# Kernel optimization log

Measured on AMD Instinct MI355X. Metric: run time of the kernel, lower is better.

The kernel has to match this reference:

```python
import jax, jax.numpy as jnp
import numpy as np

HEAD_NUM = 16
MASK_FILL = 100000.0  # source uses +1e5 on masked entries (not -inf)


def setup_inputs() -> dict:
    key = jax.random.key(0)
    k1, k2, k3, k4, k5 = jax.random.split(key, 5)
    B, S, E = 2, 2048, 1024
    scale = 0.02
    return {
        "x": jax.random.normal(k1, (B, S, E), dtype=jnp.float32),
        "W_atten": jax.random.normal(k2, (E, 3 * E), dtype=jnp.float32) * scale,
        "b_atten": jax.random.normal(k3, (3 * E,), dtype=jnp.float32) * scale,
        "W_proj": jax.random.normal(k4, (E, E), dtype=jnp.float32) * scale,
        "b_proj": jax.random.normal(k5, (E,), dtype=jnp.float32) * scale,
    }


def reference(x, W_atten, b_atten, W_proj, b_proj):
    B, S, E = x.shape
    H = HEAD_NUM
    hd = E // H
    # QKV projection: [B, S, 3E]
    qkv = x @ W_atten + b_atten
    # reshape [B, S, H, 3*hd] -> [B, H, S, 3*hd], chunk into q,k,v [B,H,S,hd]
    qkv = jnp.transpose(qkv.reshape(B, S, H, 3 * hd), (0, 2, 1, 3))
    q, k, v = jnp.split(qkv, 3, axis=-1)
    # raw scores, NO 1/sqrt(dk) scaling (faithful to source)
    w = jnp.einsum("bhqd,bhkd->bhqk", q, k)
    # causal mask applied as w*mask + (1-mask)*1e5 (faithful to source)
    mask = jnp.tril(jnp.ones((S, S), dtype=w.dtype))
    w = w * mask + (1.0 - mask) * MASK_FILL
    # softmax over dim=1 == HEAD axis (faithful to source quirk)
    w = jax.nn.softmax(w, axis=1)
    # attn_drop: identity in eval mode
    a = jnp.einsum("bhqk,bhkd->bhqd", w, v)  # [B,H,S,hd]
    a = jnp.transpose(a, (0, 2, 1, 3)).reshape(B, S, E)
    h = a @ W_proj + b_proj
    # resi_drop: identity in eval mode
    return h
```

## Files before the change

### kernel.cpp

```cpp
#include <hip/hip_runtime.h>

#define DI __device__ __forceinline__

typedef __attribute__((ext_vector_type(8))) short s16x8;
typedef __attribute__((ext_vector_type(4))) short s16x4;
typedef __attribute__((ext_vector_type(4))) float f32x4;

DI unsigned short f2bf(float f){
  unsigned u = __float_as_uint(f);
  u = (u + 0x7FFFu + ((u >> 16) & 1u)) >> 16;
  return (unsigned short)u;
}
DI float bf2f(unsigned short h){
  return __uint_as_float(((unsigned)h) << 16);
}

DI void gll16(const void* g, void* l){
  __builtin_amdgcn_global_load_lds((const __attribute__((address_space(1))) void*)g,
                                   (__attribute__((address_space(3))) void*)l, 16, 0, 0);
}

__global__ void cvt_kernel(const float* __restrict__ in, unsigned short* __restrict__ out, int n8){
  int i = blockIdx.x * blockDim.x + threadIdx.x;
  if (i >= n8) return;
  const float4* p = (const float4*)in + (size_t)i * 2;
  float4 a = p[0], b = p[1];
  s16x8 o;
  o[0] = (short)f2bf(a.x); o[1] = (short)f2bf(a.y); o[2] = (short)f2bf(a.z); o[3] = (short)f2bf(a.w);
  o[4] = (short)f2bf(b.x); o[5] = (short)f2bf(b.y); o[6] = (short)f2bf(b.z); o[7] = (short)f2bf(b.w);
  ((s16x8*)out)[i] = o;
}

__global__ void transpose_cvt(const float* __restrict__ in, unsigned short* __restrict__ out, int R, int C){
  __shared__ float t[32][33];
  int c0 = blockIdx.x * 32, r0 = blockIdx.y * 32;
  int tx = threadIdx.x, ty = threadIdx.y;
  #pragma unroll
  for (int i = 0; i < 4; i++)
    t[ty + i*8][tx] = in[(size_t)(r0 + ty + i*8) * C + c0 + tx];
  __syncthreads();
  #pragma unroll
  for (int i = 0; i < 4; i++)
    out[(size_t)(c0 + ty + i*8) * R + r0 + tx] = f2bf(t[tx][ty + i*8]);
}

template<int MODE>
__launch_bounds__(256)
__global__ void gemm_kernel(const unsigned short* __restrict__ A,
                            const unsigned short* __restrict__ Wt,
                            const float* __restrict__ bias,
                            int N,
                            unsigned short* __restrict__ qb,
                            unsigned short* __restrict__ kb,
                            unsigned short* __restrict__ vt,
                            float* __restrict__ out)
{
  const int K = 1024;
  __shared__ unsigned short As[128 * 64];
  __shared__ unsigned short Bs[128 * 64];
  int m0 = blockIdx.y * 128, n0 = blockIdx.x * 128;
  int tid = threadIdx.x;
  int lane = tid & 63, w = tid >> 6;
  int row_l = lane & 15, kgrp = lane >> 4;
  int wm = (w >> 1) * 64, wn = (w & 1) * 64;

  const unsigned short* asrc[4];
  const unsigned short* bsrc[4];
  int ldso[4];
  int chunk = (lane & 7) ^ (lane >> 3);
  #pragma unroll
  for (int c4 = 0; c4 < 4; c4++){
    int r = c4*32 + w*8 + (lane >> 3);
    asrc[c4] = A  + (size_t)(m0 + r) * K + chunk*8;
    bsrc[c4] = Wt + (size_t)(n0 + r) * K + chunk*8;
    ldso[c4] = (c4*32 + w*8) * 64;
  }
  int eA[4], eB[4];
  #pragma unroll
  for (int i = 0; i < 4; i++){
    int ra = wm + i*16 + row_l;
    eA[i] = (ra*64 + kgrp*8) ^ ((ra & 7) << 3);
    int rb = wn + i*16 + row_l;
    eB[i] = (rb*64 + kgrp*8) ^ ((rb & 7) << 3);
  }

  f32x4 acc[4][4];
  #pragma unroll
  for (int i = 0; i < 4; i++)
    #pragma unroll
    for (int j = 0; j < 4; j++)
      acc[i][j] = (f32x4){0.f, 0.f, 0.f, 0.f};

  for (int k0 = 0; k0 < K; k0 += 64){
    #pragma unroll
    for (int c4 = 0; c4 < 4; c4++){
      gll16(asrc[c4] + k0, (void*)(As + ldso[c4]));
      gll16(bsrc[c4] + k0, (void*)(Bs + ldso[c4]));
    }
    __syncthreads();
    #pragma unroll
    for (int kc = 0; kc < 2; kc++){
      s16x8 af[4], bfr[4];
      #pragma unroll
      for (int mi = 0; mi < 4; mi++)
        af[mi] = *(const s16x8*)&As[eA[mi] ^ (kc*32)];
      #pragma unroll
      for (int ni = 0; ni < 4; ni++)
        bfr[ni] = *(const s16x8*)&Bs[eB[ni] ^ (kc*32)];
      #pragma unroll
      for (int mi = 0; mi < 4; mi++)
        #pragma unroll
        for (int ni = 0; ni < 4; ni++)
          acc[mi][ni] = __builtin_amdgcn_mfma_f32_16x16x32_bf16(af[mi], bfr[ni], acc[mi][ni], 0, 0, 0);
    }
    __syncthreads();
  }

  #pragma unroll
  for (int mi = 0; mi < 4; mi++){
    #pragma unroll
    for (int ni = 0; ni < 4; ni++){
      #pragma unroll
      for (int j = 0; j < 4; j++){
        int gr = m0 + wm + mi*16 + kgrp*4 + j;
        int gc = n0 + wn + ni*16 + row_l;
        float v = acc[mi][ni][j] + bias[gc];
        if (MODE == 0){
          int h = gc / 192, cc = gc % 192;
          int b = gr >> 11, s = gr & 2047;
          unsigned short bv = f2bf(v);
          if (cc < 64){
            qb[(size_t)gr * 1024 + h*64 + cc] = bv;
          } else if (cc < 128){
            int d = cc - 64; int kt = s >> 6, kk = s & 63;
            kb[(size_t)((b*16 + h)*32 + kt) * 4096 + ((kk*64 + d) ^ ((kk & 7) << 3))] = bv;
          } else {
            int d = cc - 128; int kt = s >> 6, kk = s & 63;
            vt[(size_t)((b*16 + h)*32 + kt) * 4096 + ((d*64 + kk) ^ ((d & 7) << 3))] = bv;
          }
        } else {
          out[(size_t)gr * N + gc] = v;
        }
      }
    }
  }
}

__global__ void sufv_kernel(const unsigned short* __restrict__ vt, float* __restrict__ sufv){
  __shared__ float tot[4][64];
  int bh = blockIdx.x;
  int tid = threadIdx.x;
  int tq = tid >> 6, d = tid & 63;
  const unsigned short* base = vt + (size_t)bh * 32 * 4096;
  float s[8];
  float run = 0.f;
  for (int j = 7; j >= 0; j--){
    int t = tq*8 + j;
    float rs = 0.f;
    #pragma unroll
    for (int c = 0; c < 8; c++){
      int idx = (d*64 + c*8) ^ ((d & 7) << 3);
      s16x8 v = *(const s16x8*)&base[(size_t)t*4096 + idx];
      #pragma unroll
      for (int e = 0; e < 8; e++) rs += bf2f((unsigned short)v[e]);
    }
    run += rs; s[j] = run;
  }
  tot[tq][d] = run;
  __syncthreads();
  float carry = 0.f;
  for (int t2 = tq+1; t2 < 4; t2++) carry += tot[t2][d];
  #pragma unroll
  for (int j = 0; j < 8; j++)
    sufv[((size_t)bh*33 + tq*8 + j)*64 + d] = s[j] + carry;
  if (tid < 64) sufv[((size_t)bh*33 + 32)*64 + tid] = 0.f;
}

__launch_bounds__(256)
__global__ void dpass_kernel(const unsigned short* __restrict__ qbuf,
                             const unsigned short* __restrict__ kb,
                             float* __restrict__ invDQ)
{
  __shared__ unsigned short Kst[4][4096];
  int blk = blockIdx.x;
  int b = blk / 528, t = blk % 528;
  int qt = (int)((sqrtf(8.f*t + 1.f) - 1.f) * 0.5f);
  while ((qt+1)*(qt+2)/2 <= t) qt++;
  while (qt*(qt+1)/2 > t) qt--;
  int kt = t - qt*(qt+1)/2;

  int tid = threadIdx.x, lane = tid & 63, w = tid >> 6;
  int row_l = lane & 15, kgrp = lane >> 4;

  const unsigned short* ktb = kb + ((size_t)(b*16)*32 + kt) * 4096;
  int sgoff = (w*128 + lane)*8;

  auto stage = [&](int hh, int buf){
    const unsigned short* src = ktb + (size_t)hh * 131072;
    gll16(src + sgoff,       (void*)(&Kst[buf][0] + w*1024));
    gll16(src + sgoff + 512, (void*)(&Kst[buf][0] + w*1024 + 512));
  };

  int e0[4];
  #pragma unroll
  for (int ks = 0; ks < 4; ks++){
    int row = ks*16 + row_l;
    e0[ks] = (row*64 + kgrp*8) ^ ((row & 7) << 3);
  }

  stage(0, 0);
  stage(1, 1);

  f32x4 esum[4];
  #pragma unroll
  for (int ks = 0; ks < 4; ks++) esum[ks] = (f32x4){0.f,0.f,0.f,0.f};

  const unsigned short* qrow_p = qbuf + (size_t)(b*2048 + qt*64 + w*16 + row_l) * 1024;
  s16x8 qf0 = *(const s16x8*)&qrow_p[kgrp*8];
  s16x8 qf1 = *(const s16x8*)&qrow_p[32 + kgrp*8];

  for (int h = 0; h < 16; h++){
    s16x8 qn0, qn1;
    if (h < 15){
      qn0 = *(const s16x8*)&qrow_p[(h+1)*64 + kgrp*8];
      qn1 = *(const s16x8*)&qrow_p[(h+1)*64 + 32 + kgrp*8];
    }
    if (h + 2 < 16) stage(h+2, (h+2) & 3);
    __builtin_amdgcn_sched_barrier(0);
    if (h < 14)      asm volatile("s_waitcnt vmcnt(8)" ::: "memory");
    else if (h < 15) asm volatile("s_waitcnt vmcnt(6)" ::: "memory");
    else             asm volatile("s_waitcnt vmcnt(2)" ::: "memory");
    __builtin_amdgcn_sched_barrier(0);
    __builtin_amdgcn_s_barrier();
    __builtin_amdgcn_sched_barrier(0);

    const unsigned short* kl = &Kst[h & 3][0];
    #pragma unroll
    for (int ks = 0; ks < 4; ks++){
      s16x8 a0 = *(const s16x8*)&kl[e0[ks]];
      s16x8 a1 = *(const s16x8*)&kl[e0[ks] ^ 32];
      f32x4 sc = __builtin_amdgcn_mfma_f32_16x16x32_bf16(a0, qf0, (f32x4){0.f,0.f,0.f,0.f}, 0, 0, 0);
      sc = __builtin_amdgcn_mfma_f32_16x16x32_bf16(a1, qf1, sc, 0, 0, 0);
      #pragma unroll
      for (int j = 0; j < 4; j++) esum[ks][j] += __expf(sc[j]);
    }
    if (h < 15){ qf0 = qn0; qf1 = qn1; }
  }

  int qcol = qt*64 + w*16 + row_l;
  float* dst = invDQ + (size_t)b*4194304 + (size_t)qcol*2048 + kt*64 + kgrp*4;
  #pragma unroll
  for (int ks = 0; ks < 4; ks++){
    f32x4 rv;
    #pragma unroll
    for (int j = 0; j < 4; j++) rv[j] = 1.f / esum[ks][j];
    *(f32x4*)&dst[ks*16] = rv;
  }
}

__launch_bounds__(256)
__global__ void pv_kernel(const unsigned short* __restrict__ qbuf,
                          const unsigned short* __restrict__ kb,
                          const unsigned short* __restrict__ vt,
                          const float* __restrict__ invDQ,
                          const float* __restrict__ sufv,
                          unsigned short* __restrict__ ab,
                          float* __restrict__ pb)
{
  extern __shared__ unsigned short lds[];
  unsigned short* KstB = lds;
  unsigned short* VstB = lds + 16384;
  unsigned short* WsB  = lds + 32768;

  int blk = blockIdx.x;
  int b = blk >> 9;
  int r = blk & 511;
  int h = r >> 5;
  int r2 = r & 31;
  int i = r2 >> 1, half = r2 & 1;
  int qsm = i, qbig = 31 - i;

  int tid = threadIdx.x, lane = tid & 63, w = tid >> 6;
  int row_l = lane & 15, kgrp = lane >> 4;

  const unsigned short* KT = kb + (size_t)((b*16 + h)*32) * 4096;
  const unsigned short* VT = vt + (size_t)((b*16 + h)*32) * 4096;
  int sgoff = (w*128 + lane)*8;
  unsigned short* Wsw = WsB + w*1152;

  int eK[4];
  #pragma unroll
  for (int ks = 0; ks < 4; ks++){
    int row = ks*16 + row_l;
    eK[ks] = (row*64 + kgrp*8) ^ ((row & 7) << 3);
  }

  auto stage = [&](int kt, int buf){
    gll16(KT + (size_t)kt*4096 + sgoff,       (void*)(KstB + buf*4096 + w*1024));
    gll16(KT + (size_t)kt*4096 + sgoff + 512, (void*)(KstB + buf*4096 + w*1024 + 512));
    gll16(VT + (size_t)kt*4096 + sgoff,       (void*)(VstB + buf*4096 + w*1024));
    gll16(VT + (size_t)kt*4096 + sgoff + 512, (void*)(VstB + buf*4096 + w*1024 + 512));
  };

  auto run = [&](int qt, int k0t, int k1t, int mode){
    int q0 = qt * 64;
    int qv = q0 + w*16 + row_l;
    const unsigned short* qrow_p = qbuf + (size_t)(b*2048 + qv) * 1024 + h*64;
    s16x8 qf0 = *(const s16x8*)&qrow_p[kgrp*8];
    s16x8 qf1 = *(const s16x8*)&qrow_p[32 + kgrp*8];
    const float* ivrow = invDQ + (size_t)b*4194304 + (size_t)qv*2048 + kgrp*4;

    f32x4 pvv[4];
    #pragma unroll
    for (int d = 0; d < 4; d++) pvv[d] = (f32x4){0.f,0.f,0.f,0.f};

    stage(k0t, 0);
    f32x4 inxt[4];
    #pragma unroll
    for (int ks = 0; ks < 4; ks++) inxt[ks] = *(const f32x4*)&ivrow[k0t*64 + ks*16];
    if (k0t + 1 < k1t) stage(k0t+1, 1);

    for (int kt = k0t; kt < k1t; kt++){
      int par = (kt - k0t) & 3;
      f32x4 icur[4];
      #pragma unroll
      for (int ks = 0; ks < 4; ks++) icur[ks] = inxt[ks];
      if (kt + 1 < k1t){
        #pragma unroll
        for (int ks = 0; ks < 4; ks++) inxt[ks] = *(const f32x4*)&ivrow[(kt+1)*64 + ks*16];
      }
      if (kt + 2 < k1t) stage(kt+2, (par + 2) & 3);
      __builtin_amdgcn_sched_barrier(0);
      if (kt + 2 < k1t)      asm volatile("s_waitcnt vmcnt(16)" ::: "memory");
      else if (kt + 1 < k1t) asm volatile("s_waitcnt vmcnt(12)" ::: "memory");
      else                   asm volatile("s_waitcnt vmcnt(4)" ::: "memory");
      __builtin_amdgcn_sched_barrier(0);
      __builtin_amdgcn_s_barrier();
      __builtin_amdgcn_sched_barrier(0);

      const unsigned short* kl = KstB + par*4096;
      const unsigned short* vl = VstB + par*4096;
      f32x4 sc[4];
      #pragma unroll
      for (int ks = 0; ks < 4; ks++){
        s16x8 a0 = *(const s16x8*)&kl[eK[ks]];
        s16x8 a1 = *(const s16x8*)&kl[eK[ks] ^ 32];
        sc[ks] = __builtin_amdgcn_mfma_f32_16x16x32_bf16(a0, qf0, (f32x4){0.f,0.f,0.f,0.f}, 0, 0, 0);
        sc[ks] = __builtin_amdgcn_mfma_f32_16x16x32_bf16(a1, qf1, sc[ks], 0, 0, 0);
      }
      int kbase = kt*64 + kgrp*4;
      #pragma unroll
      for (int ks = 0; ks < 4; ks++){
        #pragma unroll
        for (int j = 0; j < 4; j++){
          float e = __expf(sc[ks][j]);
          sc[ks][j] = (kbase + ks*16 + j > qv) ? 0.0625f : e * icur[ks][j];
        }
        unsigned lo, hi;
        asm("v_cvt_pk_bf16_f32 %0, %1, %2" : "=v"(lo) : "v"(sc[ks][0]), "v"(sc[ks][1]));
        asm("v_cvt_pk_bf16_f32 %0, %1, %2" : "=v"(hi) : "v"(sc[ks][2]), "v"(sc[ks][3]));
        uint2 pk2; pk2.x = lo; pk2.y = hi;
        *(uint2*)&Wsw[row_l*72 + ks*16 + kgrp*4] = pk2;
      }
      #pragma unroll
      for (int kc = 0; kc < 2; kc++){
        s16x8 af = *(const s16x8*)&Wsw[row_l*72 + kc*32 + kgrp*8];
        #pragma unroll
        for (int dq = 0; dq < 4; dq++){
          s16x8 vf = *(const s16x8*)&vl[eK[dq] ^ (kc*32)];
          pvv[dq] = __builtin_amdgcn_mfma_f32_16x16x32_bf16(af, vf, pvv[dq], 0, 0, 0);
        }
      }
    }

    if (mode == 0){
      int tsuf = qt + 1;
      #pragma unroll
      for (int dq = 0; dq < 4; dq++){
        int d = dq*16 + row_l;
        float suf = sufv[((size_t)(b*16 + h)*33 + tsuf)*64 + d];
        #pragma unroll
        for (int j = 0; j < 4; j++){
          int qo = q0 + w*16 + kgrp*4 + j;
          ab[(size_t)(b*2048 + qo)*1024 + h*64 + d] = f2bf(pvv[dq][j] + 0.0625f * suf);
        }
      }
    } else {
      float* pr = pb + ((size_t)((b*16 + h)*16 + i)*2 + (mode - 1)) * 4096;
      #pragma unroll
      for (int dq = 0; dq < 4; dq++){
        int d = dq*16 + row_l;
        #pragma unroll
        for (int j = 0; j < 4; j++)
          pr[(w*16 + kgrp*4 + j)*64 + d] = pvv[dq][j];
      }
    }
  };

  if (half == 0){
    run(qsm, 0, i + 1, 0);
    run(qbig, 0, 16 - i, 1);
  } else {
    run(qbig, 16 - i, 32 - i, 2);
  }
}

__global__ void reduce_kernel(const float* __restrict__ pb,
                              const float* __restrict__ sufv,
                              unsigned short* __restrict__ ab)
{
  int blk = blockIdx.x;
  int b = blk >> 8, rr = blk & 255;
  int h = rr >> 4, i = rr & 15;
  int qbig = 31 - i, tsuf = 32 - i;
  int t = threadIdx.x;
  int q = t >> 2, dbase = (t & 3) * 16;
  const float* p0 = pb + ((size_t)((b*16 + h)*16 + i)*2 + 0)*4096 + q*64 + dbase;
  const float* p1 = p0 + 4096;
  const float* sf = sufv + ((size_t)(b*16 + h)*33 + tsuf)*64 + dbase;
  unsigned short* op = ab + (size_t)(b*2048 + qbig*64 + q)*1024 + h*64 + dbase;
  #pragma unroll
  for (int e = 0; e < 4; e++){
    float4 a = *(const float4*)(p0 + e*4);
    float4 bb = *(const float4*)(p1 + e*4);
    float4 s = *(const float4*)(sf + e*4);
    unsigned short o[4];
    o[0] = f2bf(a.x + bb.x + 0.0625f * s.x);
    o[1] = f2bf(a.y + bb.y + 0.0625f * s.y);
    o[2] = f2bf(a.z + bb.z + 0.0625f * s.z);
    o[3] = f2bf(a.w + bb.w + 0.0625f * s.w);
    *(s16x4*)(op + e*4) = *(s16x4*)o;
  }
}

extern "C" void kernel_launch(void* const* d_in, const int* in_sizes, int n_in,
                              void* d_out, int out_size, void* d_ws, size_t ws_size,
                              hipStream_t stream) {
  (void)in_sizes; (void)n_in; (void)out_size; (void)ws_size;
  const float* x  = (const float*)d_in[0];
  const float* Wa = (const float*)d_in[1];
  const float* ba = (const float*)d_in[2];
  const float* Wp = (const float*)d_in[3];
  const float* bp = (const float*)d_in[4];
  float* out = (float*)d_out;

  char* ws = (char*)d_ws;
  size_t off = 0;
  auto alloc = [&](size_t bytes) -> void* {
    void* p = ws + off;
    off += (bytes + 255) & ~(size_t)255;
    return p;
  };
  float* pbuf          = (float*)alloc((size_t)16*1024*1024);
  unsigned short* xb   = (unsigned short*)((char*)pbuf);
  unsigned short* WaT  = (unsigned short*)((char*)pbuf + (size_t)4096*1024*2);
  unsigned short* WpT  = (unsigned short*)alloc((size_t)1024*1024*2);
  unsigned short* qbuf = (unsigned short*)alloc((size_t)4096*1024*2);
  unsigned short* ktile= (unsigned short*)alloc((size_t)4096*1024*2);
  unsigned short* vtile= (unsigned short*)alloc((size_t)4096*1024*2);
  unsigned short* abuf = (unsigned short*)alloc((size_t)4096*1024*2);
  float* invDQ         = (float*)alloc((size_t)2*2048*2048*4);
  float* sufv          = (float*)alloc((size_t)32*33*64*4);

  cvt_kernel<<<2048, 256, 0, stream>>>(x, xb, 4096*1024/8);
  transpose_cvt<<<dim3(3072/32, 1024/32), dim3(32, 8), 0, stream>>>(Wa, WaT, 1024, 3072);
  transpose_cvt<<<dim3(1024/32, 1024/32), dim3(32, 8), 0, stream>>>(Wp, WpT, 1024, 1024);

  gemm_kernel<0><<<dim3(24, 32), 256, 0, stream>>>(xb, WaT, ba, 3072, qbuf, ktile, vtile, nullptr);

  sufv_kernel<<<32, 256, 0, stream>>>(vtile, sufv);

  dpass_kernel<<<1056, 256, 0, stream>>>(qbuf, ktile, invDQ);

  static int smem_set = 0;
  size_t smem = (size_t)(16384 + 16384 + 4608) * sizeof(unsigned short);
  if (!smem_set) {
    hipFuncSetAttribute(reinterpret_cast<const void*>(pv_kernel),
                        hipFuncAttributeMaxDynamicSharedMemorySize, (int)smem);
    smem_set = 1;
  }
  pv_kernel<<<1024, 256, smem, stream>>>(qbuf, ktile, vtile, invDQ, sufv, abuf, pbuf);

  reduce_kernel<<<512, 256, 0, stream>>>(pbuf, sufv, abuf);

  gemm_kernel<1><<<dim3(8, 32), 256, 0, stream>>>(abuf, WpT, bp, 1024, nullptr, nullptr, nullptr, out);
}
```

Baseline: 177.7 us.

## Shrink pv LDS to double buffer, remap block order, use BM=64 for proj GEMM

The PV kernel drops from a 4-deep to a 2-deep K/V staging ring in static shared memory, which cuts LDS use to allow more resident blocks, at the cost of less prefetch depth. Block indices for the dpass and pv kernels are permuted so that blocks with different workloads or heads are spread across XCDs/CUs, and dpass enumerates tiles in kt-major triangular order. The output projection GEMM is templated on BM and uses 64-row tiles, doubling its block count to fill more CUs with only 256 output tiles available.

Measured after the change: 182.8 us. 1.03x slower.

```diff
diff --git a/kernel.cpp b/kernel.cpp
--- a/kernel.cpp
+++ b/kernel.cpp
@@ -44,7 +44,7 @@
     out[(size_t)(c0 + ty + i*8) * R + r0 + tx] = f2bf(t[tx][ty + i*8]);
 }
 
-template<int MODE>
+template<int MODE, int BM>
 __launch_bounds__(256)
 __global__ void gemm_kernel(const unsigned short* __restrict__ A,
                             const unsigned short* __restrict__ Wt,
@@ -55,60 +55,71 @@
                             unsigned short* __restrict__ vt,
                             float* __restrict__ out)
 {
+  constexpr int MI = BM / 32;
+  constexpr int AC = BM / 32;
   const int K = 1024;
-  __shared__ unsigned short As[128 * 64];
+  __shared__ unsigned short As[BM * 64];
   __shared__ unsigned short Bs[128 * 64];
-  int m0 = blockIdx.y * 128, n0 = blockIdx.x * 128;
+  int m0 = blockIdx.y * BM, n0 = blockIdx.x * 128;
   int tid = threadIdx.x;
   int lane = tid & 63, w = tid >> 6;
   int row_l = lane & 15, kgrp = lane >> 4;
-  int wm = (w >> 1) * 64, wn = (w & 1) * 64;
-
-  const unsigned short* asrc[4];
+  int wm = (w >> 1) * (MI * 16), wn = (w & 1) * 64;
+
+  const unsigned short* asrc[AC];
   const unsigned short* bsrc[4];
-  int ldso[4];
+  int ldsoA[AC], ldsoB[4];
   int chunk = (lane & 7) ^ (lane >> 3);
+  #pragma unroll
+  for (int c4 = 0; c4 < AC; c4++){
+    int r = c4*32 + w*8 + (lane >> 3);
+    asrc[c4] = A + (size_t)(m0 + r) * K + chunk*8;
+    ldsoA[c4] = (c4*32 + w*8) * 64;
+  }
   #pragma unroll
   for (int c4 = 0; c4 < 4; c4++){
     int r = c4*32 + w*8 + (lane >> 3);
-    asrc[c4] = A  + (size_t)(m0 + r) * K + chunk*8;
     bsrc[c4] = Wt + (size_t)(n0 + r) * K + chunk*8;
-    ldso[c4] = (c4*32 + w*8) * 64;
-  }
-  int eA[4], eB[4];
-  #pragma unroll
-  for (int i = 0; i < 4; i++){
+    ldsoB[c4] = (c4*32 + w*8) * 64;
+  }
+  int eA[MI], eB[4];
+  #pragma unroll
+  for (int i = 0; i < MI; i++){
     int ra = wm + i*16 + row_l;
     eA[i] = (ra*64 + kgrp*8) ^ ((ra & 7) << 3);
+  }
+  #pragma unroll
+  for (int i = 0; i < 4; i++){
     int rb = wn + i*16 + row_l;
     eB[i] = (rb*64 + kgrp*8) ^ ((rb & 7) << 3);
   }
 
-  f32x4 acc[4][4];
-  #pragma unroll
-  for (int i = 0; i < 4; i++)
+  f32x4 acc[MI][4];
+  #pragma unroll
+  for (int i = 0; i < MI; i++)
     #pragma unroll
     for (int j = 0; j < 4; j++)
       acc[i][j] = (f32x4){0.f, 0.f, 0.f, 0.f};
 
   for (int k0 = 0; k0 < K; k0 += 64){
     #pragma unroll
-    for (int c4 = 0; c4 < 4; c4++){
-      gll16(asrc[c4] + k0, (void*)(As + ldso[c4]));
-      gll16(bsrc[c4] + k0, (void*)(Bs + ldso[c4]));
-    }
+    for (int c4 = 0; c4 < AC; c4++)
+      gll16(asrc[c4] + k0, (void*)(As + ldsoA[c4]));
+    #pragma unroll
+    for (int c4 = 0; c4 < 4; c4++)
+      gll16(bsrc[c4] + k0, (void*)(Bs + ldsoB[c4]));
     __syncthreads();
     #pragma unroll
     for (int kc = 0; kc < 2; kc++){
-      s16x8 af[4], bfr[4];
-      #pragma unroll
-      for (int mi = 0; mi < 4; mi++)
+      s16x8 af[MI], bfr[4];
+      #pragma unroll
+      for (int mi = 0; mi < MI; mi++)
         af[mi] = *(const s16x8*)&As[eA[mi] ^ (kc*32)];
       #pragma unroll
       for (int ni = 0; ni < 4; ni++)
         bfr[ni] = *(const s16x8*)&Bs[eB[ni] ^ (kc*32)];
       #pragma unroll
-      for (int mi = 0; mi < 4; mi++)
+      for (int mi = 0; mi < MI; mi++)
         #pragma unroll
         for (int ni = 0; ni < 4; ni++)
           acc[mi][ni] = __builtin_amdgcn_mfma_f32_16x16x32_bf16(af[mi], bfr[ni], acc[mi][ni], 0, 0, 0);
@@ -117,7 +128,7 @@
   }
 
   #pragma unroll
-  for (int mi = 0; mi < 4; mi++){
+  for (int mi = 0; mi < MI; mi++){
     #pragma unroll
     for (int ni = 0; ni < 4; ni++){
       #pragma unroll
@@ -182,12 +193,13 @@
                              float* __restrict__ invDQ)
 {
   __shared__ unsigned short Kst[4][4096];
-  int blk = blockIdx.x;
+  int bid = blockIdx.x;
+  int blk = (bid & 7) * 132 + (bid >> 3);
   int b = blk / 528, t = blk % 528;
-  int qt = (int)((sqrtf(8.f*t + 1.f) - 1.f) * 0.5f);
-  while ((qt+1)*(qt+2)/2 <= t) qt++;
-  while (qt*(qt+1)/2 > t) qt--;
-  int kt = t - qt*(qt+1)/2;
+  int kt = (int)(32.5f - sqrtf(1056.25f - 2.f*t));
+  while (kt*(65-kt)/2 > t) kt--;
+  while ((kt+1)*(64-kt)/2 <= t) kt++;
+  int qt = kt + (t - kt*(65-kt)/2);
 
   int tid = threadIdx.x, lane = tid & 63, w = tid >> 6;
   int row_l = lane & 15, kgrp = lane >> 4;
@@ -267,12 +279,11 @@
                           unsigned short* __restrict__ ab,
                           float* __restrict__ pb)
 {
-  extern __shared__ unsigned short lds[];
-  unsigned short* KstB = lds;
-  unsigned short* VstB = lds + 16384;
-  unsigned short* WsB  = lds + 32768;
-
-  int blk = blockIdx.x;
+  __shared__ unsigned short Kst[2][4096];
+  __shared__ unsigned short Vst[2][4096];
+  __shared__ unsigned short Wsh[4][1152];
+
+  int blk = ((blockIdx.x & 7) << 7) + (blockIdx.x >> 3);
   int b = blk >> 9;
   int r = blk & 511;
   int h = r >> 5;
@@ -286,7 +297,7 @@
   const unsigned short* KT = kb + (size_t)((b*16 + h)*32) * 4096;
   const unsigned short* VT = vt + (size_t)((b*16 + h)*32) * 4096;
   int sgoff = (w*128 + lane)*8;
-  unsigned short* Wsw = WsB + w*1152;
+  unsigned short* Wsw = &Wsh[w][0];
 
   int eK[4];
   #pragma unroll
@@ -296,10 +307,10 @@
   }
 
   auto stage = [&](int kt, int buf){
-    gll16(KT + (size_t)kt*4096 + sgoff,       (void*)(KstB + buf*4096 + w*1024));
-    gll16(KT + (size_t)kt*4096 + sgoff + 512, (void*)(KstB + buf*4096 + w*1024 + 512));
-    gll16(VT + (size_t)kt*4096 + sgoff,       (void*)(VstB + buf*4096 + w*1024));
-    gll16(VT + (size_t)kt*4096 + sgoff + 512, (void*)(VstB + buf*4096 + w*1024 + 512));
+    gll16(KT + (size_t)kt*4096 + sgoff,       (void*)(&Kst[buf][0] + w*1024));
+    gll16(KT + (size_t)kt*4096 + sgoff + 512, (void*)(&Kst[buf][0] + w*1024 + 512));
+    gll16(VT + (size_t)kt*4096 + sgoff,       (void*)(&Vst[buf][0] + w*1024));
+    gll16(VT + (size_t)kt*4096 + sgoff + 512, (void*)(&Vst[buf][0] + w*1024 + 512));
   };
 
   auto run = [&](int qt, int k0t, int k1t, int mode){
@@ -314,32 +325,33 @@
     #pragma unroll
     for (int d = 0; d < 4; d++) pvv[d] = (f32x4){0.f,0.f,0.f,0.f};
 
+    __syncthreads();
     stage(k0t, 0);
     f32x4 inxt[4];
     #pragma unroll
     for (int ks = 0; ks < 4; ks++) inxt[ks] = *(const f32x4*)&ivrow[k0t*64 + ks*16];
-    if (k0t + 1 < k1t) stage(k0t+1, 1);
 
     for (int kt = k0t; kt < k1t; kt++){
-      int par = (kt - k0t) & 3;
+      int bufc = (kt - k0t) & 1;
+      bool nx = (kt + 1 < k1t);
+      __builtin_amdgcn_s_barrier();
+      if (nx) stage(kt+1, bufc ^ 1);
       f32x4 icur[4];
       #pragma unroll
       for (int ks = 0; ks < 4; ks++) icur[ks] = inxt[ks];
-      if (kt + 1 < k1t){
+      if (nx){
         #pragma unroll
         for (int ks = 0; ks < 4; ks++) inxt[ks] = *(const f32x4*)&ivrow[(kt+1)*64 + ks*16];
       }
-      if (kt + 2 < k1t) stage(kt+2, (par + 2) & 3);
       __builtin_amdgcn_sched_barrier(0);
-      if (kt + 2 < k1t)      asm volatile("s_waitcnt vmcnt(16)" ::: "memory");
-      else if (kt + 1 < k1t) asm volatile("s_waitcnt vmcnt(12)" ::: "memory");
-      else                   asm volatile("s_waitcnt vmcnt(4)" ::: "memory");
+      if (nx) asm volatile("s_waitcnt vmcnt(12)" ::: "memory");
+      else    asm volatile("s_waitcnt vmcnt(4)" ::: "memory");
       __builtin_amdgcn_sched_barrier(0);
       __builtin_amdgcn_s_barrier();
       __builtin_amdgcn_sched_barrier(0);
 
-      const unsigned short* kl = KstB + par*4096;
-      const unsigned short* vl = VstB + par*4096;
+      const unsigned short* kl = &Kst[bufc][0];
+      const unsigned short* vl = &Vst[bufc][0];
       f32x4 sc[4];
       #pragma unroll
       for (int ks = 0; ks < 4; ks++){
@@ -466,22 +478,15 @@
   transpose_cvt<<<dim3(3072/32, 1024/32), dim3(32, 8), 0, stream>>>(Wa, WaT, 1024, 3072);
   transpose_cvt<<<dim3(1024/32, 1024/32), dim3(32, 8), 0, stream>>>(Wp, WpT, 1024, 1024);
 
-  gemm_kernel<0><<<dim3(24, 32), 256, 0, stream>>>(xb, WaT, ba, 3072, qbuf, ktile, vtile, nullptr);
+  gemm_kernel<0,128><<<dim3(24, 32), 256, 0, stream>>>(xb, WaT, ba, 3072, qbuf, ktile, vtile, nullptr);
 
   sufv_kernel<<<32, 256, 0, stream>>>(vtile, sufv);
 
   dpass_kernel<<<1056, 256, 0, stream>>>(qbuf, ktile, invDQ);
 
-  static int smem_set = 0;
-  size_t smem = (size_t)(16384 + 16384 + 4608) * sizeof(unsigned short);
-  if (!smem_set) {
-    hipFuncSetAttribute(reinterpret_cast<const void*>(pv_kernel),
-                        hipFuncAttributeMaxDynamicSharedMemorySize, (int)smem);
-    smem_set = 1;
-  }
-  pv_kernel<<<1024, 256, smem, stream>>>(qbuf, ktile, vtile, invDQ, sufv, abuf, pbuf);
+  pv_kernel<<<1024, 256, 0, stream>>>(qbuf, ktile, vtile, invDQ, sufv, abuf, pbuf);
 
   reduce_kernel<<<512, 256, 0, stream>>>(pbuf, sufv, abuf);
 
-  gemm_kernel<1><<<dim3(8, 32), 256, 0, stream>>>(abuf, WpT, bp, 1024, nullptr, nullptr, nullptr, out);
-}
+  gemm_kernel<1,64><<<dim3(1024/128, 4096/64), 256, 0, stream>>>(abuf, WpT, bp, 1024, nullptr, nullptr, nullptr, out);
+}
```
